# Kernel tuning notes

Hardware: AMD Instinct MI355X
Metric: run time of the kernel (lower is better)

Reference implementation:

```python
import jax, jax.numpy as jnp
import numpy as np

T = 2_097_152  # number of daily timesteps
S_INIT = 0.0   # initial store fraction (s_init in module)


def setup_inputs() -> dict:
    key = jax.random.key(0)
    k1, _ = jax.random.split(key)
    # columns: P (precipitation), E (potential evapotranspiration), mm/day scale
    x = jax.random.uniform(k1, (T, 2), dtype=jnp.float32) * 10.0
    x1 = jnp.full((1,), 350.0, dtype=jnp.float32)  # production-store capacity (mm)
    return {"x": x, "x1": x1}


def reference(x, x1):
    x1s = x1[0]
    P = x[:, 0]
    E = x[:, 1]
    p_n = jnp.maximum(P - E, 0.0)  # net precipitation
    e_n = jnp.maximum(E - P, 0.0)  # net evapotranspiration

    def step(s_store, pe):
        pn_t, en_t = pe
        tp = jnp.tanh(pn_t / x1s)
        te = jnp.tanh(en_t / x1s)
        r = s_store / x1s
        p_s = x1s * (1.0 - r ** 2) * tp / (1.0 + r * tp)
        e_s = s_store * (2.0 - r) * te / (1.0 + (1.0 - r) * te)
        s_store = s_store + p_s - e_s
        perc = s_store * (1.0 - (1.0 + (4.0 / 9.0 * s_store / x1s) ** 4) ** (-0.25))
        s_store = s_store - perc
        return s_store, (p_s, perc)

    s0 = jnp.float32(S_INIT) * x1s
    _, (p_s, perc) = jax.lax.scan(step, s0, (p_n, e_n))

    # out: [T, 6] = [P, E, p_n, e_n, p_s, perc]
    out = jnp.concatenate(
        [x, p_n[:, None], e_n[:, None], p_s[:, None], perc[:, None]], axis=1
    )
    mu = out.mean(axis=0)
    sigma = out.std(axis=0, ddof=1)  # torch.std uses Bessel correction
    return (out - mu) / sigma
```

## Files before the change

kernel.cpp:

```cpp
#include <hip/hip_runtime.h>


#define T_TOTAL   (1 << 21)
#define C_CHUNKS  (T_TOTAL / 16)
#define NCOARSE   32
#define NTAIL     128
#define THREADS   256
#define NBLOCKS   (C_CHUNKS / THREADS)
#define NSTAGE4   2376
#define LDSN      4768
#define NWIN      287
#define X4MAX     (T_TOTAL / 2 - 1)
#define C49       0.44444445f

#define OFF_SP    0
#define OFF_MUSIG 49152
#define OFF_SIDE  49664

#define SWZ(w) ((w) ^ (((w) >> 4) & 31))
#define RD(Sb, mm) (*(const float2*)(lbase + ((Sb) ^ ((mm) << 3))))

#define CL(v) fminf(fmaxf((v), 0.0f), rmax)

#define DRIFT(RV, C, OUT)                                                  \
    {                                                                      \
        float rr_ = (RV);                                                  \
        float d_ = fmaf(rr_, fmaf(rr_, fmaf(rr_, (C).w, (C).z), (C).y), (C).x); \
        float y_  = rr_ * C49;                                             \
        float y2_ = y_ * y_;                                               \
        float u_  = y2_ * y2_;                                             \
        float pl_ = fmaf(u_, fmaf(u_, 1.875f, -2.5f), 4.0f);               \
        OUT = d_ - (rr_ * u_) * pl_;                                       \
    }

#define CSTEP(C)                                                           \
    {                                                                      \
        float k1_, k2_;                                                    \
        DRIFT(r, C, k1_)                                                   \
        float sm_ = CL(r + k1_);                                           \
        DRIFT(sm_, C, k2_)                                                 \
        r = CL(fmaf(0.5f, k1_ + k2_, r));                                  \
    }

#define WLD(j) make_float4(cA[kp + (j)], cB[kp + (j)], cC[kp + (j)], cD[kp + (j)])

#define CGRP_R(OFF)                                                        \
    CSTEP(c0) c0 = WLD((OFF) + 8);  CSTEP(c1) c1 = WLD((OFF) + 9);         \
    CSTEP(c2) c2 = WLD((OFF) + 10); CSTEP(c3) c3 = WLD((OFF) + 11);        \
    CSTEP(c4) c4 = WLD((OFF) + 12); CSTEP(c5) c5 = WLD((OFF) + 13);        \
    CSTEP(c6) c6 = WLD((OFF) + 14); CSTEP(c7) c7 = WLD((OFF) + 15);
#define CGRP_L                                                             \
    CSTEP(c0) CSTEP(c1) CSTEP(c2) CSTEP(c3)                                \
    CSTEP(c4) CSTEP(c5) CSTEP(c6) CSTEP(c7)

#define FSTEP(a, b2)                                                       \
    {                                                                      \
        float m_  = fmaf(-0.5f, (b2), (a));                       \
        float rn_ = r + fmaf(r, fmaf(r, -m_, -(b2)), (a));                 \
        float y_  = rn_ * C49; float y2_ = y_ * y_; float u_ = y2_ * y2_;  \
        float pl_ = fmaf(u_, -0.15625f, 0.25f);                            \
        r = rn_ - (rn_ * u_) * pl_;                                        \
    }

#define ESTEP(a, b2, PS, PC)                                               \
    {                                                                      \
        float b_   = 0.5f * (b2);                                          \
        float tp_  = (a) * fmaf((a) * (a), -0.33333334f, 1.0f);            \
        float te_  = b_ * fmaf(b_ * b_, -0.33333334f, 1.0f);               \
        float q1_  = fmaf(-r, tp_, 1.0f);                        \
        float dp_  = (tp_ * fmaf(-r, r, 1.0f)) * q1_;                      \
        float omr_ = 1.0f - r;                                             \
        float q2_  = fmaf(-te_, omr_, 1.0f);                     \
        float de_  = ((r * (2.0f - r)) * te_) * q2_;                       \
        float rn_  = r + (dp_ - de_);                                      \
        float y_   = rn_ * C49; float y2_ = y_ * y_; float u_ = y2_ * y2_; \
        float pl_  = fmaf(u_, fmaf(u_, 0.1171875f, -0.15625f), 0.25f);     \
        float pcr_ = (rn_ * u_) * pl_;                                     \
        r = rn_ - pcr_;                                                    \
        PS = x1s * dp_;                                                    \
        PC = x1s * pcr_;                                                   \
    }

#define FQ(RN, mm)                                                         \
    FSTEP(RN.x, RN.y)                                                      \
    RN = ((mm) < 12) ? RD(Sc, (mm) + 4) : RD(Sn, (mm) - 12);

#define EPAIR2(RA, RB, m0)                                                 \
    {                                                                      \
        float psA, pcA, psB, pcB;                                          \
        ESTEP(RA.x, RA.y, psA, pcA)                                        \
        ESTEP(RB.x, RB.y, psB, pcB)                                        \
        if (SIDE) {                                                        \
            *(float4*)(side + 2 * (size_t)(t0 + (m0))) =                   \
                make_float4(psA, pcA, psB, pcB);                           \
        } else {                                                           \
            *(float2*)(out + 6 * (size_t)(t0 + (m0)) + 4)  = make_float2(psA, pcA); \
            *(float2*)(out + 6 * (size_t)(t0 + (m0)) + 10) = make_float2(psB, pcB); \
        }                                                                  \
        sum4 += psA + psB; sq4 = fmaf(psA, psA, sq4); sq4 = fmaf(psB, psB, sq4); \
        sum5 += pcA + pcB; sq5 = fmaf(pcA, pcA, sq5); sq5 = fmaf(pcB, pcB, sq5); \
        if ((m0) < 12) { RA = RD(Se, (m0) + 4); RB = RD(Se, (m0) + 5); }   \
    }

template <bool SIDE>
__global__ __launch_bounds__(256, 2) void scan_kernel(const float4* __restrict__ x4,
                                                      const float* __restrict__ x1p,
                                                      float* __restrict__ out,
                                                      float* __restrict__ side,
                                                      double* __restrict__ sp) {
    __shared__ float2 plane[LDSN];
    __shared__ float cA[NWIN + 1], cB[NWIN + 1], cC[NWIN + 1], cD[NWIN + 1];
    __shared__ double red[4][12];

    const float x1s    = x1p[0];
    const float inv_x1 = 1.0f / x1s;
    const float inv2x  = 2.0f * inv_x1;
    const float rmax   = 320.0f * inv_x1;
    const int k  = blockIdx.x * 256 + threadIdx.x;
    const int kp = threadIdx.x;
    const char* lbase = (const char*)plane;

    float s0 = 0, s1 = 0, s2c = 0, s3 = 0, q0 = 0, q1 = 0, q2 = 0, q3 = 0;
    {
        const int g0 = 2048 * blockIdx.x - 320;
        for (int j = 0; j < 10; ++j) {
            int ts = threadIdx.x + 256 * j;
            if (ts < NSTAGE4) {
                int g4 = g0 + ts;
                float4 v = x4[min(max(g4, 0), X4MAX)];
                float pn0 = fmaxf(v.x - v.y, 0.0f), en0 = fmaxf(v.y - v.x, 0.0f);
                float pn1 = fmaxf(v.z - v.w, 0.0f), en1 = fmaxf(v.w - v.z, 0.0f);
                if (g4 < 0) { pn0 = en0 = pn1 = en1 = 0.0f; }
                plane[SWZ(2 * ts)]     = make_float2(pn0 * inv_x1, en0 * inv2x);
                plane[SWZ(2 * ts + 1)] = make_float2(pn1 * inv_x1, en1 * inv2x);
                if (ts >= 320 && ts < 2368) {
                    s0 += v.x + v.z; q0 = fmaf(v.x, v.x, q0); q0 = fmaf(v.z, v.z, q0);
                    s1 += v.y + v.w; q1 = fmaf(v.y, v.y, q1); q1 = fmaf(v.w, v.w, q1);
                    s2c += pn0 + pn1; q2 = fmaf(pn0, pn0, q2); q2 = fmaf(pn1, pn1, q2);
                    s3 += en0 + en1; q3 = fmaf(en0, en0, q3); q3 = fmaf(en1, en1, q3);
                }
            }
        }
    }
    __syncthreads();

    for (int wl = threadIdx.x; wl < NWIN; wl += 256) {
        const int Sw = SWZ(16 * wl) << 3;
        float Sa = 0, Sa2 = 0, Sb = 0, Sb2 = 0;
#pragma unroll
        for (int mm = 0; mm < 16; ++mm) {
            float2 p = RD(Sw, mm);
            Sa += p.x; Sa2 = fmaf(p.x, p.x, Sa2);
            Sb += p.y; Sb2 = fmaf(p.y, p.y, Sb2);
        }
        float Tp = Sa, Qp = Sa2, Te = 0.5f * Sb, Qe = 0.25f * Sb2;
        cA[wl] = Tp;
        cB[wl] = 2.0f * (Qe - Te) - Qp;
        cC[wl] = Te - Tp - 3.0f * Qe;
        cD[wl] = Qp + Qe;
    }
    __syncthreads();

    float4 c0 = WLD(0), c1 = WLD(1), c2 = WLD(2), c3 = WLD(3),
           c4 = WLD(4), c5 = WLD(5), c6 = WLD(6), c7 = WLD(7);
    float r = 0.0f;
    CGRP_R(0) CGRP_R(8) CGRP_R(16) CGRP_L

    float2 r0, r1, r2, r3;
    {
        const int S0 = SWZ(16 * kp + 512) << 3;
        r0 = RD(S0, 0); r1 = RD(S0, 1); r2 = RD(S0, 2); r3 = RD(S0, 3);
    }
#pragma unroll 1
    for (int B = 0; B < NTAIL; B += 16) {
        const int W0 = 16 * kp + 512 + B;
        const int Sc = SWZ(W0) << 3;
        const int Sn = SWZ(W0 + 16) << 3;
        FQ(r0, 0)  FQ(r1, 1)  FQ(r2, 2)  FQ(r3, 3)
        FQ(r0, 4)  FQ(r1, 5)  FQ(r2, 6)  FQ(r3, 7)
        FQ(r0, 8)  FQ(r1, 9)  FQ(r2, 10) FQ(r3, 11)
        FQ(r0, 12) FQ(r1, 13) FQ(r2, 14) FQ(r3, 15)
    }

    float sum4 = 0, sum5 = 0, sq4 = 0, sq5 = 0;
    const int t0 = 16 * k;
    const int Se = SWZ(16 * kp + 512 + NTAIL) << 3;
    EPAIR2(r0, r1, 0)  EPAIR2(r2, r3, 2)
    EPAIR2(r0, r1, 4)  EPAIR2(r2, r3, 6)
    EPAIR2(r0, r1, 8)  EPAIR2(r2, r3, 10)
    EPAIR2(r0, r1, 12) EPAIR2(r2, r3, 14)

    double vv[12] = {s0, s1, s2c, s3, sum4, sum5,
                     q0, q1, q2, q3, sq4, sq5};
    const int wid = threadIdx.x >> 6, lane = threadIdx.x & 63;
#pragma unroll
    for (int c = 0; c < 12; ++c) {
        double val = vv[c];
        for (int off = 32; off > 0; off >>= 1) val += __shfl_down(val, off, 64);
        if (lane == 0) red[wid][c] = val;
    }
    __syncthreads();
    if (threadIdx.x < 12) {
        int c = threadIdx.x;
        sp[c * 512 + blockIdx.x] = red[0][c] + red[1][c] + red[2][c] + red[3][c];
    }
}

__global__ __launch_bounds__(256) void finalize_kernel(const double* __restrict__ sp,
                                                       float* __restrict__ musig) {
    __shared__ double red[12][4];
    const int t = threadIdx.x, lane = t & 63, wid = t >> 6;
#pragma unroll
    for (int c = 0; c < 12; ++c) {
        double v = sp[c * 512 + t] + sp[c * 512 + 256 + t];
        for (int off = 32; off > 0; off >>= 1) v += __shfl_down(v, off, 64);
        if (lane == 0) red[c][wid] = v;
    }
    __syncthreads();
    if (t < 6) {
        double sum = red[t][0] + red[t][1] + red[t][2] + red[t][3];
        double sq  = red[6 + t][0] + red[6 + t][1] + red[6 + t][2] + red[6 + t][3];
        double n = (double)T_TOTAL;
        double mu = sum / n;
        double var = (sq - sum * sum / n) / (n - 1.0);
        musig[t] = (float)mu;
        musig[6 + t] = (float)(1.0 / sqrt(var));
    }
}

template <bool SIDE>
__global__ __launch_bounds__(256) void normalize_kernel(const float4* __restrict__ xp4,
                                                        const float4* __restrict__ side4,
                                                        float* __restrict__ out,
                                                        const float* __restrict__ musig) {
    float mu[6], is[6];
#pragma unroll
    for (int c = 0; c < 6; ++c) { mu[c] = musig[c]; is[c] = musig[6 + c]; }

    int idx = blockIdx.x * blockDim.x + threadIdx.x;
    int stride = gridDim.x * blockDim.x;
    for (int p = idx; p < T_TOTAL / 2; p += stride) {
        float4 xv = xp4[p];
        float* o = out + 12 * (size_t)p;
        float4 sv;
        if (SIDE) {
            sv = side4[p];
        } else {
            float2 a = *(const float2*)(o + 4);
            float2 b = *(const float2*)(o + 10);
            sv = make_float4(a.x, a.y, b.x, b.y);
        }
        float pn0 = fmaxf(xv.x - xv.y, 0.0f), en0 = fmaxf(xv.y - xv.x, 0.0f);
        float pn1 = fmaxf(xv.z - xv.w, 0.0f), en1 = fmaxf(xv.w - xv.z, 0.0f);
        float4 o0 = {(xv.x - mu[0]) * is[0], (xv.y - mu[1]) * is[1],
                     (pn0 - mu[2]) * is[2], (en0 - mu[3]) * is[3]};
        float4 o1 = {(sv.x - mu[4]) * is[4], (sv.y - mu[5]) * is[5],
                     (xv.z - mu[0]) * is[0], (xv.w - mu[1]) * is[1]};
        float4 o2 = {(pn1 - mu[2]) * is[2], (en1 - mu[3]) * is[3],
                     (sv.z - mu[4]) * is[4], (sv.w - mu[5]) * is[5]};
        *(float4*)(o + 0) = o0;
        *(float4*)(o + 4) = o1;
        *(float4*)(o + 8) = o2;
    }
}

extern "C" void kernel_launch(void* const* d_in, const int* in_sizes, int n_in,
                              void* d_out, int out_size, void* d_ws, size_t ws_size,
                              hipStream_t stream) {
    const float4* x4 = (const float4*)d_in[0];
    const float* x1 = (const float*)d_in[1];
    float* out = (float*)d_out;
    char* ws = (char*)d_ws;
    double* sp = (double*)(ws + OFF_SP);
    float* musig = (float*)(ws + OFF_MUSIG);
    float* side = (float*)(ws + OFF_SIDE);

    const bool use_side = ws_size >= (size_t)OFF_SIDE + (size_t)T_TOTAL * 8;

    if (use_side) {
        scan_kernel<true><<<NBLOCKS, THREADS, 0, stream>>>(x4, x1, out, side, sp);
        finalize_kernel<<<1, 256, 0, stream>>>(sp, musig);
        normalize_kernel<true><<<2048, 256, 0, stream>>>(x4, (const float4*)side, out, musig);
    } else {
        scan_kernel<false><<<NBLOCKS, THREADS, 0, stream>>>(x4, x1, out, side, sp);
        finalize_kernel<<<1, 256, 0, stream>>>(sp, musig);
        normalize_kernel<false><<<2048, 256, 0, stream>>>(x4, (const float4*)side, out, musig);
    }
}
```

Measured before the change: 48.96 us.

## Fuse scan, statistics finalize and normalize into one cooperative kernel

Merges the scan, finalize and normalize launches into a single cooperative-groups kernel that uses a grid-wide sync after writing per-block partial sums. Each block keeps its p_s/perc results in LDS, so the side buffer is neither written to nor read back from global memory, and two kernel launches go away. The cost is an extra 32KB of LDS per block, which may reduce occupancy, plus the requirement that all 512 blocks be co-resident for the grid sync. The old no-workspace fallback path is removed.

```diff
diff --git a/kernel.cpp b/kernel.cpp
--- a/kernel.cpp
+++ b/kernel.cpp
@@ -1,9 +1,11 @@
 #include <hip/hip_runtime.h>
+#include <hip/hip_cooperative_groups.h>
+
+namespace cg = cooperative_groups;
 
 
 #define T_TOTAL   (1 << 21)
 #define C_CHUNKS  (T_TOTAL / 16)
-#define NCOARSE   32
 #define NTAIL     128
 #define THREADS   256
 #define NBLOCKS   (C_CHUNKS / THREADS)
@@ -19,7 +21,6 @@
 
 #define SWZ(w) ((w) ^ (((w) >> 4) & 31))
 #define RD(Sb, mm) (*(const float2*)(lbase + ((Sb) ^ ((mm) << 3))))
-
 #define CL(v) fminf(fmaxf((v), 0.0f), rmax)
 
 #define DRIFT(RV, C, OUT)                                                  \
@@ -85,38 +86,32 @@
     FSTEP(RN.x, RN.y)                                                      \
     RN = ((mm) < 12) ? RD(Sc, (mm) + 4) : RD(Sn, (mm) - 12);
 
-#define EPAIR2(RA, RB, m0)                                                 \
+#define EPAIR2F(RA, RB, m0)                                                \
     {                                                                      \
         float psA, pcA, psB, pcB;                                          \
         ESTEP(RA.x, RA.y, psA, pcA)                                        \
         ESTEP(RB.x, RB.y, psB, pcB)                                        \
-        if (SIDE) {                                                        \
-            *(float4*)(side + 2 * (size_t)(t0 + (m0))) =                   \
-                make_float4(psA, pcA, psB, pcB);                           \
-        } else {                                                           \
-            *(float2*)(out + 6 * (size_t)(t0 + (m0)) + 4)  = make_float2(psA, pcA); \
-            *(float2*)(out + 6 * (size_t)(t0 + (m0)) + 10) = make_float2(psB, pcB); \
-        }                                                                  \
+        psperc[SWZ(eb + (m0))]     = make_float2(psA, pcA);                \
+        psperc[SWZ(eb + (m0) + 1)] = make_float2(psB, pcB);                \
         sum4 += psA + psB; sq4 = fmaf(psA, psA, sq4); sq4 = fmaf(psB, psB, sq4); \
         sum5 += pcA + pcB; sq5 = fmaf(pcA, pcA, sq5); sq5 = fmaf(pcB, pcB, sq5); \
         if ((m0) < 12) { RA = RD(Se, (m0) + 4); RB = RD(Se, (m0) + 5); }   \
     }
 
-template <bool SIDE>
-__global__ __launch_bounds__(256, 2) void scan_kernel(const float4* __restrict__ x4,
-                                                      const float* __restrict__ x1p,
-                                                      float* __restrict__ out,
-                                                      float* __restrict__ side,
-                                                      double* __restrict__ sp) {
+__global__ __launch_bounds__(256, 2) void fused_kernel(const float4* __restrict__ x4,
+                                                       const float* __restrict__ x1p,
+                                                       float* __restrict__ out,
+                                                       double* __restrict__ sp) {
     __shared__ float2 plane[LDSN];
+    __shared__ float2 psperc[4096];
     __shared__ float cA[NWIN + 1], cB[NWIN + 1], cC[NWIN + 1], cD[NWIN + 1];
     __shared__ double red[4][12];
+    __shared__ float sh[12];
 
     const float x1s    = x1p[0];
     const float inv_x1 = 1.0f / x1s;
     const float inv2x  = 2.0f * inv_x1;
     const float rmax   = 320.0f * inv_x1;
-    const int k  = blockIdx.x * 256 + threadIdx.x;
     const int kp = threadIdx.x;
     const char* lbase = (const char*)plane;
 
@@ -183,6 +178,169 @@
     }
 
     float sum4 = 0, sum5 = 0, sq4 = 0, sq5 = 0;
+    const int eb = 16 * kp;
+    const int Se = SWZ(16 * kp + 512 + NTAIL) << 3;
+    EPAIR2F(r0, r1, 0)  EPAIR2F(r2, r3, 2)
+    EPAIR2F(r0, r1, 4)  EPAIR2F(r2, r3, 6)
+    EPAIR2F(r0, r1, 8)  EPAIR2F(r2, r3, 10)
+    EPAIR2F(r0, r1, 12) EPAIR2F(r2, r3, 14)
+
+    double vv[12] = {s0, s1, s2c, s3, sum4, sum5,
+                     q0, q1, q2, q3, sq4, sq5};
+    const int wid = threadIdx.x >> 6, lane = threadIdx.x & 63;
+#pragma unroll
+    for (int c = 0; c < 12; ++c) {
+        double val = vv[c];
+        for (int off = 32; off > 0; off >>= 1) val += __shfl_down(val, off, 64);
+        if (lane == 0) red[wid][c] = val;
+    }
+    __syncthreads();
+    if (threadIdx.x < 12) {
+        int c = threadIdx.x;
+        sp[c * 512 + blockIdx.x] = red[0][c] + red[1][c] + red[2][c] + red[3][c];
+    }
+
+    cg::this_grid().sync();
+
+    {
+        const int t = threadIdx.x;
+#pragma unroll
+        for (int c = 0; c < 12; ++c) {
+            double v = sp[c * 512 + t] + sp[c * 512 + 256 + t];
+            for (int off = 32; off > 0; off >>= 1) v += __shfl_down(v, off, 64);
+            if (lane == 0) red[wid][c] = v;
+        }
+        __syncthreads();
+        if (t < 6) {
+            double sum = red[0][t] + red[1][t] + red[2][t] + red[3][t];
+            double sq  = red[0][6 + t] + red[1][6 + t] + red[2][6 + t] + red[3][6 + t];
+            double n = (double)T_TOTAL;
+            double mu = sum / n;
+            double var = (sq - sum * sum / n) / (n - 1.0);
+            sh[t] = (float)mu;
+            sh[6 + t] = (float)(1.0 / sqrt(var));
+        }
+        __syncthreads();
+    }
+
+    {
+        float mu[6], is[6];
+#pragma unroll
+        for (int c = 0; c < 6; ++c) { mu[c] = sh[c]; is[c] = sh[6 + c]; }
+        float4* out4 = (float4*)out;
+        const int pb = 2048 * blockIdx.x;
+        const size_t ob = 6144ull * blockIdx.x;
+#pragma unroll 1
+        for (int i = 0; i < 8; ++i) {
+            int pl = i * 256 + threadIdx.x;
+            float4 xv = x4[pb + pl];
+            int lr = 2 * pl;
+            float2 P0 = psperc[SWZ(lr)];
+            float2 P1 = psperc[SWZ(lr + 1)];
+            float pn0 = fmaxf(xv.x - xv.y, 0.0f), en0 = fmaxf(xv.y - xv.x, 0.0f);
+            float pn1 = fmaxf(xv.z - xv.w, 0.0f), en1 = fmaxf(xv.w - xv.z, 0.0f);
+            float4* o = out4 + ob + 3 * (size_t)pl;
+            o[0] = make_float4((xv.x - mu[0]) * is[0], (xv.y - mu[1]) * is[1],
+                               (pn0 - mu[2]) * is[2], (en0 - mu[3]) * is[3]);
+            o[1] = make_float4((P0.x - mu[4]) * is[4], (P0.y - mu[5]) * is[5],
+                               (xv.z - mu[0]) * is[0], (xv.w - mu[1]) * is[1]);
+            o[2] = make_float4((pn1 - mu[2]) * is[2], (en1 - mu[3]) * is[3],
+                               (P1.x - mu[4]) * is[4], (P1.y - mu[5]) * is[5]);
+        }
+    }
+}
+
+#define EPAIR2(RA, RB, m0)                                                 \
+    {                                                                      \
+        float psA, pcA, psB, pcB;                                          \
+        ESTEP(RA.x, RA.y, psA, pcA)                                        \
+        ESTEP(RB.x, RB.y, psB, pcB)                                        \
+        *(float4*)(side + 2 * (size_t)(t0 + (m0))) =                       \
+            make_float4(psA, pcA, psB, pcB);                               \
+        sum4 += psA + psB; sq4 = fmaf(psA, psA, sq4); sq4 = fmaf(psB, psB, sq4); \
+        sum5 += pcA + pcB; sq5 = fmaf(pcA, pcA, sq5); sq5 = fmaf(pcB, pcB, sq5); \
+        if ((m0) < 12) { RA = RD(Se, (m0) + 4); RB = RD(Se, (m0) + 5); }   \
+    }
+
+__global__ __launch_bounds__(256, 2) void scan_kernel(const float4* __restrict__ x4,
+                                                      const float* __restrict__ x1p,
+                                                      float* __restrict__ side,
+                                                      double* __restrict__ sp) {
+    __shared__ float2 plane[LDSN];
+    __shared__ float cA[NWIN + 1], cB[NWIN + 1], cC[NWIN + 1], cD[NWIN + 1];
+    __shared__ double red[4][12];
+
+    const float x1s    = x1p[0];
+    const float inv_x1 = 1.0f / x1s;
+    const float inv2x  = 2.0f * inv_x1;
+    const float rmax   = 320.0f * inv_x1;
+    const int k  = blockIdx.x * 256 + threadIdx.x;
+    const int kp = threadIdx.x;
+    const char* lbase = (const char*)plane;
+
+    float s0 = 0, s1 = 0, s2c = 0, s3 = 0, q0 = 0, q1 = 0, q2 = 0, q3 = 0;
+    {
+        const int g0 = 2048 * blockIdx.x - 320;
+        for (int j = 0; j < 10; ++j) {
+            int ts = threadIdx.x + 256 * j;
+            if (ts < NSTAGE4) {
+                int g4 = g0 + ts;
+                float4 v = x4[min(max(g4, 0), X4MAX)];
+                float pn0 = fmaxf(v.x - v.y, 0.0f), en0 = fmaxf(v.y - v.x, 0.0f);
+                float pn1 = fmaxf(v.z - v.w, 0.0f), en1 = fmaxf(v.w - v.z, 0.0f);
+                if (g4 < 0) { pn0 = en0 = pn1 = en1 = 0.0f; }
+                plane[SWZ(2 * ts)]     = make_float2(pn0 * inv_x1, en0 * inv2x);
+                plane[SWZ(2 * ts + 1)] = make_float2(pn1 * inv_x1, en1 * inv2x);
+                if (ts >= 320 && ts < 2368) {
+                    s0 += v.x + v.z; q0 = fmaf(v.x, v.x, q0); q0 = fmaf(v.z, v.z, q0);
+                    s1 += v.y + v.w; q1 = fmaf(v.y, v.y, q1); q1 = fmaf(v.w, v.w, q1);
+                    s2c += pn0 + pn1; q2 = fmaf(pn0, pn0, q2); q2 = fmaf(pn1, pn1, q2);
+                    s3 += en0 + en1; q3 = fmaf(en0, en0, q3); q3 = fmaf(en1, en1, q3);
+                }
+            }
+        }
+    }
+    __syncthreads();
+
+    for (int wl = threadIdx.x; wl < NWIN; wl += 256) {
+        const int Sw = SWZ(16 * wl) << 3;
+        float Sa = 0, Sa2 = 0, Sb = 0, Sb2 = 0;
+#pragma unroll
+        for (int mm = 0; mm < 16; ++mm) {
+            float2 p = RD(Sw, mm);
+            Sa += p.x; Sa2 = fmaf(p.x, p.x, Sa2);
+            Sb += p.y; Sb2 = fmaf(p.y, p.y, Sb2);
+        }
+        float Tp = Sa, Qp = Sa2, Te = 0.5f * Sb, Qe = 0.25f * Sb2;
+        cA[wl] = Tp;
+        cB[wl] = 2.0f * (Qe - Te) - Qp;
+        cC[wl] = Te - Tp - 3.0f * Qe;
+        cD[wl] = Qp + Qe;
+    }
+    __syncthreads();
+
+    float4 c0 = WLD(0), c1 = WLD(1), c2 = WLD(2), c3 = WLD(3),
+           c4 = WLD(4), c5 = WLD(5), c6 = WLD(6), c7 = WLD(7);
+    float r = 0.0f;
+    CGRP_R(0) CGRP_R(8) CGRP_R(16) CGRP_L
+
+    float2 r0, r1, r2, r3;
+    {
+        const int S0 = SWZ(16 * kp + 512) << 3;
+        r0 = RD(S0, 0); r1 = RD(S0, 1); r2 = RD(S0, 2); r3 = RD(S0, 3);
+    }
+#pragma unroll 1
+    for (int B = 0; B < NTAIL; B += 16) {
+        const int W0 = 16 * kp + 512 + B;
+        const int Sc = SWZ(W0) << 3;
+        const int Sn = SWZ(W0 + 16) << 3;
+        FQ(r0, 0)  FQ(r1, 1)  FQ(r2, 2)  FQ(r3, 3)
+        FQ(r0, 4)  FQ(r1, 5)  FQ(r2, 6)  FQ(r3, 7)
+        FQ(r0, 8)  FQ(r1, 9)  FQ(r2, 10) FQ(r3, 11)
+        FQ(r0, 12) FQ(r1, 13) FQ(r2, 14) FQ(r3, 15)
+    }
+
+    float sum4 = 0, sum5 = 0, sq4 = 0, sq5 = 0;
     const int t0 = 16 * k;
     const int Se = SWZ(16 * kp + 512 + NTAIL) << 3;
     EPAIR2(r0, r1, 0)  EPAIR2(r2, r3, 2)
@@ -228,7 +386,6 @@
     }
 }
 
-template <bool SIDE>
 __global__ __launch_bounds__(256) void normalize_kernel(const float4* __restrict__ xp4,
                                                         const float4* __restrict__ side4,
                                                         float* __restrict__ out,
@@ -242,14 +399,7 @@
     for (int p = idx; p < T_TOTAL / 2; p += stride) {
         float4 xv = xp4[p];
         float* o = out + 12 * (size_t)p;
-        float4 sv;
-        if (SIDE) {
-            sv = side4[p];
-        } else {
-            float2 a = *(const float2*)(o + 4);
-            float2 b = *(const float2*)(o + 10);
-            sv = make_float4(a.x, a.y, b.x, b.y);
-        }
+        float4 sv = side4[p];
         float pn0 = fmaxf(xv.x - xv.y, 0.0f), en0 = fmaxf(xv.y - xv.x, 0.0f);
         float pn1 = fmaxf(xv.z - xv.w, 0.0f), en1 = fmaxf(xv.w - xv.z, 0.0f);
         float4 o0 = {(xv.x - mu[0]) * is[0], (xv.y - mu[1]) * is[1],
@@ -275,15 +425,17 @@
     float* musig = (float*)(ws + OFF_MUSIG);
     float* side = (float*)(ws + OFF_SIDE);
 
-    const bool use_side = ws_size >= (size_t)OFF_SIDE + (size_t)T_TOTAL * 8;
-
-    if (use_side) {
-        scan_kernel<true><<<NBLOCKS, THREADS, 0, stream>>>(x4, x1, out, side, sp);
+    int coop = 0;
+    hipDeviceGetAttribute(&coop, hipDeviceAttributeCooperativeLaunch, 0);
+    const bool big_ws = ws_size >= (size_t)OFF_SIDE + (size_t)T_TOTAL * 8;
+
+    if (coop) {
+        void* args[] = {(void*)&x4, (void*)&x1, (void*)&out, (void*)&sp};
+        hipLaunchCooperativeKernel((void*)fused_kernel, dim3(NBLOCKS),
+                                   dim3(THREADS), args, 0, stream);
+    } else if (big_ws) {
+        scan_kernel<<<NBLOCKS, THREADS, 0, stream>>>(x4, x1, side, sp);
         finalize_kernel<<<1, 256, 0, stream>>>(sp, musig);
-        normalize_kernel<true><<<2048, 256, 0, stream>>>(x4, (const float4*)side, out, musig);
-    } else {
-        scan_kernel<false><<<NBLOCKS, THREADS, 0, stream>>>(x4, x1, out, side, sp);
-        finalize_kernel<<<1, 256, 0, stream>>>(sp, musig);
-        normalize_kernel<false><<<2048, 256, 0, stream>>>(x4, (const float4*)side, out, musig);
+        normalize_kernel<<<2048, 256, 0, stream>>>(x4, (const float4*)side, out, musig);
     }
 }
```

New measurement: 89.91 us. 83.6% more time.
